# Kernel tuning notes

Hardware: AMD Instinct MI355X
Metric: run time of the kernel (lower is better)

## Reference

```python
import jax, jax.numpy as jnp
import numpy as np

NUM_HEADS = 12
HEAD_DIM = 64


def _rotate_half(x):
    x1, x2 = jnp.split(x, 2, axis=-1)
    return jnp.concatenate([-x2, x1], axis=-1)


def setup_inputs() -> dict:
    key = jax.random.key(0)
    ks = jax.random.split(key, 5)
    B, S, H = 4, 2048, 768
    x = jax.random.normal(ks[0], (B, S, H), dtype=jnp.float32)
    # rope tables per (batch, position, head_dim)
    pos = jnp.arange(S, dtype=jnp.float32)[:, None]
    inv = 1.0 / (10000.0 ** (jnp.arange(0, HEAD_DIM, 2, dtype=jnp.float32) / HEAD_DIM))
    ang = pos * inv[None, :]  # [S, hd/2]
    ang = jnp.concatenate([ang, ang], axis=-1)  # [S, hd]
    cos = jnp.broadcast_to(jnp.cos(ang)[None], (B, S, HEAD_DIM)).astype(jnp.float32)
    sin = jnp.broadcast_to(jnp.sin(ang)[None], (B, S, HEAD_DIM)).astype(jnp.float32)
    Wqkv = jax.random.normal(ks[1], (3 * H, H), dtype=jnp.float32) * 0.02
    Wo = jax.random.normal(ks[2], (H, H), dtype=jnp.float32) * 0.02
    return {"x": x, "cos": cos, "sin": sin, "Wqkv": Wqkv, "Wo": Wo, "window": 64}


def reference(x, cos, sin, Wqkv, Wo, window):
    B, S, H = x.shape
    nh, hd = NUM_HEADS, HEAD_DIM
    scale = hd ** -0.5
    qkv = jnp.einsum('bsh,oh->bso', x, Wqkv)  # [B,S,3H]
    qkv = qkv.reshape(B, S, 3, nh, hd)
    q = qkv[:, :, 0].transpose(0, 2, 1, 3)  # [B,nh,S,hd]
    k = qkv[:, :, 1].transpose(0, 2, 1, 3)
    v = qkv[:, :, 2].transpose(0, 2, 1, 3)
    # RoPE in float32, cos/sin broadcast over heads: [B,1,S,hd]
    c = cos[:, None].astype(jnp.float32)
    s = sin[:, None].astype(jnp.float32)
    qf, kf = q.astype(jnp.float32), k.astype(jnp.float32)
    q = (qf * c + _rotate_half(qf) * s).astype(q.dtype)
    k = (kf * c + _rotate_half(kf) * s).astype(k.dtype)
    scores = jnp.einsum('bhqd,bhkd->bhqk', q, k) * scale
    idx = jnp.arange(S)
    band = jnp.abs(idx[:, None] - idx[None, :]) <= window  # sliding-window mask
    scores = jnp.where(band[None, None], scores, -jnp.inf)
    probs = jax.nn.softmax(scores, axis=-1)
    y = jnp.einsum('bhqk,bhkd->bhqd', probs, v)  # [B,nh,S,hd]
    y = y.transpose(0, 2, 1, 3).reshape(B, S, H)
    return jnp.einsum('bsh,oh->bso', y, Wo)
```

## Files before the change

### kernel.cpp

```cpp
#include <hip/hip_runtime.h>


typedef __attribute__((ext_vector_type(8))) _Float16 f16x8;
typedef __attribute__((ext_vector_type(4))) float    f32x4;

#define BDIM 4
#define SDIM 2048
#define HDIM 768
#define NH   12
#define HD   64
#define NQKV 2304
#define MROWS 8192

__device__ __forceinline__ void gload16(const void* g, void* l) {
    __builtin_amdgcn_global_load_lds(
        (__attribute__((address_space(1))) void*)(g),
        (__attribute__((address_space(3))) void*)(l),
        16, 0, 0);
}

__global__ __launch_bounds__(256) void cvt_f32_f16(
    const float* __restrict__ src, _Float16* __restrict__ dst, int n8)
{
    int i = blockIdx.x * 256 + threadIdx.x;
    if (i >= n8) return;
    const float4* s4 = (const float4*)src + (long)i * 2;
    float4 a = s4[0], b = s4[1];
    f16x8 o;
    o[0] = (_Float16)a.x; o[1] = (_Float16)a.y;
    o[2] = (_Float16)a.z; o[3] = (_Float16)a.w;
    o[4] = (_Float16)b.x; o[5] = (_Float16)b.y;
    o[6] = (_Float16)b.z; o[7] = (_Float16)b.w;
    *((f16x8*)dst + i) = o;
}

template <int EPI>
__global__ __launch_bounds__(256) void gemm_kernel(
    const _Float16* __restrict__ A,
    const _Float16* __restrict__ Bt,
    float* __restrict__ C,
    const float* __restrict__ cosp,
    const float* __restrict__ sinp,
    _Float16* __restrict__ qh,
    _Float16* __restrict__ kh,
    _Float16* __restrict__ vh,
    int M, int N, int K)
{
    __shared__ __align__(16) _Float16 lsA[2][128 * 32];
    __shared__ __align__(16) _Float16 lsB[2][128 * 32];

    int nTn = N >> 7;
    int nwg = gridDim.x;
    int bid = blockIdx.x;
    int wg = bid;
    if ((nwg & 7) == 0) {
        int cpx = nwg >> 3;
        wg = (bid & 7) * cpx + (bid >> 3);
    }
    int tm = wg / nTn, tn = wg % nTn;
    int m0 = tm << 7, n0 = tn << 7;

    int tid  = threadIdx.x;
    int lane = tid & 63;
    int w    = tid >> 6;
    int wr   = w >> 1, wc = w & 1;
    int l15  = lane & 15, lk = lane >> 4;

    f32x4 acc[4][4] = {};

    int srow = tid >> 2;
    int scol = (tid & 3) << 3;
    const _Float16* ga0 = A  + (long)(m0 + srow) * K + scol;
    const _Float16* gb0 = Bt + (long)(n0 + srow) * K + scol;
    const long gstep = (long)64 * K;

    const int NK = K >> 5;

    {
        gload16(ga0,         &lsA[0][tid * 8]);
        gload16(ga0 + gstep, &lsA[0][tid * 8 + 2048]);
        gload16(gb0,         &lsB[0][tid * 8]);
        gload16(gb0 + gstep, &lsB[0][tid * 8 + 2048]);
    }
    __syncthreads();

    int cur = 0;
    for (int it = 0; it < NK; ++it) {
        if (it + 1 < NK) {
            const _Float16* ga = ga0 + (it + 1) * 32;
            const _Float16* gb = gb0 + (it + 1) * 32;
            int nb = cur ^ 1;
            gload16(ga,         &lsA[nb][tid * 8]);
            gload16(ga + gstep, &lsA[nb][tid * 8 + 2048]);
            gload16(gb,         &lsB[nb][tid * 8]);
            gload16(gb + gstep, &lsB[nb][tid * 8 + 2048]);
        }

        f16x8 af[4], bfr[4];
#pragma unroll
        for (int m = 0; m < 4; ++m)
            af[m] = *(const f16x8*)&lsA[cur][(wr * 64 + m * 16 + l15) * 32 + lk * 8];
#pragma unroll
        for (int n = 0; n < 4; ++n)
            bfr[n] = *(const f16x8*)&lsB[cur][(wc * 64 + n * 16 + l15) * 32 + lk * 8];
#pragma unroll
        for (int m = 0; m < 4; ++m)
#pragma unroll
            for (int n = 0; n < 4; ++n)
                acc[m][n] = __builtin_amdgcn_mfma_f32_16x16x32_f16(
                    af[m], bfr[n], acc[m][n], 0, 0, 0);

        __syncthreads();
        cur ^= 1;
    }

    if (EPI == 0) {
#pragma unroll
        for (int m = 0; m < 4; ++m)
#pragma unroll
            for (int n = 0; n < 4; ++n)
#pragma unroll
                for (int j = 0; j < 4; ++j) {
                    int gr = m0 + wr * 64 + m * 16 + lk * 4 + j;
                    int gc = n0 + wc * 64 + n * 16 + l15;
                    C[(long)gr * N + gc] = acc[m][n][j];
                }
    } else {
        int ht = (n0 >> 6) + wc;
        int t  = ht / NH;
        int h  = ht - t * NH;
        int b  = m0 >> 11;
        long base_bh = ((long)(b * NH + h)) * SDIM;
#pragma unroll
        for (int m = 0; m < 4; ++m) {
#pragma unroll
            for (int j = 0; j < 4; ++j) {
                int gr = m0 + wr * 64 + m * 16 + lk * 4 + j;
                int s  = gr & (SDIM - 1);
                if (t == 2) {
#pragma unroll
                    for (int n = 0; n < 4; ++n) {
                        int d = n * 16 + l15;
                        vh[(base_bh + s) * HD + d] = (_Float16)acc[m][n][j];
                    }
                } else {
                    float vals[4];
#pragma unroll
                    for (int n = 0; n < 4; ++n) vals[n] = acc[m][n][j];
#pragma unroll
                    for (int n = 0; n < 4; ++n) {
                        int d = n * 16 + l15;
                        float cc = cosp[(long)gr * HD + d];
                        float ss = sinp[(long)gr * HD + d];
                        float pv = (n < 2) ? -vals[n + 2] : vals[n - 2];
                        float o  = vals[n] * cc + pv * ss;
                        long oidx = (base_bh + s) * HD + d;
                        if (t == 0) qh[oidx] = (_Float16)o;
                        else        kh[oidx] = (_Float16)o;
                    }
                }
            }
        }
    }
}

#define SSTR 200
#define PSTR 200
__global__ __launch_bounds__(256) void attn_mfma(
    const _Float16* __restrict__ qh,
    const _Float16* __restrict__ kh,
    const _Float16* __restrict__ vh,
    _Float16* __restrict__ yh)
{
    __shared__ __align__(16) _Float16 lsVT[64 * SSTR];
    __shared__ __align__(16) _Float16 lsP [64 * PSTR];

    int bid = blockIdx.x;
    int qt  = bid & 31;
    int bh  = bid >> 5;
    int q0  = qt << 6;
    int k0  = q0 - 64;
    int tid = threadIdx.x;
    int lane = tid & 63;
    int w = tid >> 6;
    int l15 = lane & 15, lg = lane >> 4;

    const _Float16* Qb = qh + (long)bh * SDIM * HD;
    const _Float16* Kb = kh + (long)bh * SDIM * HD;
    const _Float16* Vb = vh + (long)bh * SDIM * HD;

#pragma unroll
    for (int c = 0; c < 3; ++c) {
        int rk = c * 64 + lane;
        int s  = k0 + rk;
        s = s < 0 ? 0 : (s >= SDIM ? SDIM - 1 : s);
        const f16x8* vr = (const f16x8*)(Vb + (long)s * HD + w * 16);
        f16x8 v0 = vr[0], v1 = vr[1];
#pragma unroll
        for (int e = 0; e < 8; ++e) {
            lsVT[(w * 16 + e)     * SSTR + rk] = v0[e];
            lsVT[(w * 16 + 8 + e) * SSTR + rk] = v1[e];
        }
    }

    int qrow = q0 + w * 16 + l15;
    const f16x8* qp = (const f16x8*)(Qb + (long)qrow * HD + lg * 8);
    f16x8 qa0 = qp[0];
    f16x8 qa1 = qp[4];

    float sums[4] = {0.f, 0.f, 0.f, 0.f};
    int iqb = w * 16 + lg * 4;
#pragma unroll 4
    for (int kt = 0; kt < 12; ++kt) {
        int krow = k0 + kt * 16 + l15;
        int kcl = krow < 0 ? 0 : (krow >= SDIM ? SDIM - 1 : krow);
        const f16x8* kp = (const f16x8*)(Kb + (long)kcl * HD + lg * 8);
        f16x8 kb0 = kp[0], kb1 = kp[4];
        f32x4 acc = {0.f, 0.f, 0.f, 0.f};
        acc = __builtin_amdgcn_mfma_f32_16x16x32_f16(qa0, kb0, acc, 0, 0, 0);
        acc = __builtin_amdgcn_mfma_f32_16x16x32_f16(qa1, kb1, acc, 0, 0, 0);
        int jk = kt * 16 + l15;
        bool kin = (krow >= 0) && (krow < SDIM);
#pragma unroll
        for (int j = 0; j < 4; ++j) {
            int i = iqb + j;
            bool valid = kin && (jk >= i) && (jk <= i + 128);
            float p = valid ? __expf(acc[j] * 0.125f) : 0.f;
            sums[j] += p;
            lsP[(w * 16 + lg * 4 + j) * PSTR + jk] = (_Float16)p;
        }
    }

#pragma unroll
    for (int m = 1; m < 16; m <<= 1) {
#pragma unroll
        for (int j = 0; j < 4; ++j)
            sums[j] += __shfl_xor(sums[j], m, 64);
    }
    float inv[4];
#pragma unroll
    for (int j = 0; j < 4; ++j) inv[j] = 1.f / sums[j];

    __syncthreads();

    f32x4 accy[4] = {};
    const _Float16* prow = &lsP[(w * 16 + l15) * PSTR + lg * 8];
#pragma unroll
    for (int kc = 0; kc < 6; ++kc) {
        f16x8 pa = *(const f16x8*)(prow + kc * 32);
#pragma unroll
        for (int dt = 0; dt < 4; ++dt) {
            f16x8 vb = *(const f16x8*)&lsVT[(dt * 16 + l15) * SSTR + kc * 32 + lg * 8];
            accy[dt] = __builtin_amdgcn_mfma_f32_16x16x32_f16(pa, vb, accy[dt], 0, 0, 0);
        }
    }

    int b = bh / NH, h = bh - (bh / NH) * NH;
    long outbase = ((long)b * SDIM) * HDIM + (long)h * HD;
#pragma unroll
    for (int dt = 0; dt < 4; ++dt) {
#pragma unroll
        for (int j = 0; j < 4; ++j) {
            int srow = q0 + w * 16 + lg * 4 + j;
            yh[outbase + (long)srow * HDIM + dt * 16 + l15] =
                (_Float16)(accy[dt][j] * inv[j]);
        }
    }
}

extern "C" void kernel_launch(void* const* d_in, const int* in_sizes, int n_in,
                              void* d_out, int out_size, void* d_ws, size_t ws_size,
                              hipStream_t stream)
{
    const float* x    = (const float*)d_in[0];
    const float* cosp = (const float*)d_in[1];
    const float* sinp = (const float*)d_in[2];
    const float* Wqkv = (const float*)d_in[3];
    const float* Wo   = (const float*)d_in[4];
    float* out = (float*)d_out;

    char* ws = (char*)d_ws;
    _Float16* xh    = (_Float16*)(ws);
    _Float16* wqkvh = (_Float16*)(ws + 12582912);
    _Float16* woh   = (_Float16*)(ws + 16121856);
    _Float16* qh    = (_Float16*)(ws + 17301504);
    _Float16* kh    = (_Float16*)(ws + 29884416);
    _Float16* vh    = (_Float16*)(ws + 42467328);
    _Float16* yh    = (_Float16*)(ws + 55050240);

    cvt_f32_f16<<<(MROWS * HDIM / 8 + 255) / 256, 256, 0, stream>>>(x, xh, MROWS * HDIM / 8);
    cvt_f32_f16<<<(NQKV * HDIM / 8 + 255) / 256, 256, 0, stream>>>(Wqkv, wqkvh, NQKV * HDIM / 8);
    cvt_f32_f16<<<(HDIM * HDIM / 8 + 255) / 256, 256, 0, stream>>>(Wo, woh, HDIM * HDIM / 8);

    {
        dim3 grid((MROWS / 128) * (NQKV / 128));
        gemm_kernel<1><<<grid, 256, 0, stream>>>(
            xh, wqkvh, nullptr, cosp, sinp, qh, kh, vh, MROWS, NQKV, HDIM);
    }

    {
        dim3 grid(BDIM * NH * (SDIM / 64));
        attn_mfma<<<grid, 256, 0, stream>>>(qh, kh, vh, yh);
    }

    {
        dim3 grid((MROWS / 128) * (HDIM / 128));
        gemm_kernel<0><<<grid, 256, 0, stream>>>(
            yh, woh, out, nullptr, nullptr, nullptr, nullptr, nullptr,
            MROWS, HDIM, HDIM);
    }
}
```

Baseline: 118.1 us.

## Prefetch two k-tiles ahead in GEMM with fine-grained vmcnt waits

The GEMM main loop now issues global-to-LDS loads two iterations ahead. Once the current tile's fragments are in registers, it refills the buffer that was just read, and uses explicit s_waitcnt vmcnt/lgkmcnt plus raw barriers in place of __syncthreads. The aim is to hide global load latency behind the MFMA work and avoid draining every outstanding load at each barrier. It relies on hand-counted vmcnt values matching the four loads per stage, and it adds a second barrier per iteration.

```diff
diff --git a/kernel.cpp b/kernel.cpp
--- a/kernel.cpp
+++ b/kernel.cpp
@@ -73,29 +73,27 @@
     const _Float16* ga0 = A  + (long)(m0 + srow) * K + scol;
     const _Float16* gb0 = Bt + (long)(n0 + srow) * K + scol;
     const long gstep = (long)64 * K;
+    _Float16* laP[2] = { &lsA[0][tid * 8], &lsA[1][tid * 8] };
+    _Float16* lbP[2] = { &lsB[0][tid * 8], &lsB[1][tid * 8] };
 
     const int NK = K >> 5;
 
-    {
-        gload16(ga0,         &lsA[0][tid * 8]);
-        gload16(ga0 + gstep, &lsA[0][tid * 8 + 2048]);
-        gload16(gb0,         &lsB[0][tid * 8]);
-        gload16(gb0 + gstep, &lsB[0][tid * 8 + 2048]);
-    }
-    __syncthreads();
+#define STAGE(buf, t) do {                                   \
+        const _Float16* ga_ = ga0 + (t) * 32;                \
+        const _Float16* gb_ = gb0 + (t) * 32;                \
+        gload16(ga_,         laP[buf]);                      \
+        gload16(ga_ + gstep, laP[buf] + 2048);               \
+        gload16(gb_,         lbP[buf]);                      \
+        gload16(gb_ + gstep, lbP[buf] + 2048);               \
+    } while (0)
+
+    STAGE(0, 0);
+    STAGE(1, 1);
+    asm volatile("s_waitcnt vmcnt(4)" ::: "memory");
+    __builtin_amdgcn_s_barrier();
 
     int cur = 0;
     for (int it = 0; it < NK; ++it) {
-        if (it + 1 < NK) {
-            const _Float16* ga = ga0 + (it + 1) * 32;
-            const _Float16* gb = gb0 + (it + 1) * 32;
-            int nb = cur ^ 1;
-            gload16(ga,         &lsA[nb][tid * 8]);
-            gload16(ga + gstep, &lsA[nb][tid * 8 + 2048]);
-            gload16(gb,         &lsB[nb][tid * 8]);
-            gload16(gb + gstep, &lsB[nb][tid * 8 + 2048]);
-        }
-
         f16x8 af[4], bfr[4];
 #pragma unroll
         for (int m = 0; m < 4; ++m)
@@ -103,6 +101,12 @@
 #pragma unroll
         for (int n = 0; n < 4; ++n)
             bfr[n] = *(const f16x8*)&lsB[cur][(wc * 64 + n * 16 + l15) * 32 + lk * 8];
+
+        asm volatile("s_waitcnt lgkmcnt(0)" ::: "memory");
+        __builtin_amdgcn_s_barrier();
+
+        if (it + 2 < NK) STAGE(cur, it + 2);
+
 #pragma unroll
         for (int m = 0; m < 4; ++m)
 #pragma unroll
@@ -110,9 +114,16 @@
                 acc[m][n] = __builtin_amdgcn_mfma_f32_16x16x32_f16(
                     af[m], bfr[n], acc[m][n], 0, 0, 0);
 
-        __syncthreads();
+        if (it + 1 < NK) {
+            if (it + 2 < NK)
+                asm volatile("s_waitcnt vmcnt(4)" ::: "memory");
+            else
+                asm volatile("s_waitcnt vmcnt(0)" ::: "memory");
+            __builtin_amdgcn_s_barrier();
+        }
         cur ^= 1;
     }
+#undef STAGE
 
     if (EPI == 0) {
 #pragma unroll
```

After: 114.6 us. -3.0%, faster.
